# Kernel tuning notes

Measured on AMD Instinct MI355X. Metric: run time of the kernel, lower is better.

The kernel has to match this reference:

```python
import jax, jax.numpy as jnp
import numpy as np

H, W, BS, CIN = 224, 608, 1, 128
CLS = (16, 12, 10)
PAD = (0, 2, 3)
C12 = CLS[0] * CLS[1]            # 192
C123 = C12 * CLS[2]              # 1920
SUPER = 384
CFACT = C123 // SUPER            # 5
PAD_PROJ = 0.1


def _p(key, shape):
    return jax.random.normal(key, shape, dtype=jnp.float32) * 0.05


def setup_inputs() -> dict:
    key = jax.random.key(0)
    ks = iter(jax.random.split(key, 32))
    d = {"x_in": jax.random.normal(next(ks), (BS, CIN, H, W), dtype=jnp.float32)}
    # stage-1: grouped 1x1 convs (groups=height -> one [out,in] matmul per image line)
    for i, (ci, co) in enumerate([(32, 32), (32, 32), (32, CLS[0] + 2 * PAD[0])]):
        d[f"w1_{i}"] = _p(next(ks), (H, co, ci))
        d[f"b1_{i}"] = _p(next(ks), (H, co))
    # stage-2: CondMul tables indexed by line*16 + stage-1 class
    for i, (ci, co) in enumerate([(32, 32), (32, 32), (32, CLS[1] + 2 * PAD[1])]):
        d[f"w2_{i}"] = _p(next(ks), (H * CLS[0], ci, co))
        d[f"b2_{i}"] = _p(next(ks), (H * CLS[0], co))
    # stage-3: CondMul tables indexed by line*192 + stage-12 class
    for i, (ci, co) in enumerate([(32, 32), (32, 32), (32, CLS[2] + 2 * PAD[2])]):
        d[f"w3_{i}"] = _p(next(ks), (H * C12, ci, co))
        d[f"b3_{i}"] = _p(next(ks), (H * C12, co))
    d["wr0"] = _p(next(ks), (H * SUPER, 32, 32))
    d["br0"] = _p(next(ks), (H * SUPER, 32))
    d["wr1"] = _p(next(ks), (H * C123, 32, 1))
    d["br1"] = _p(next(ks), (H * C123, 1))
    return d


def _condmul(x, inds, w, b):
    # CondMul: y[n] = x[n] @ w[inds[n]] + b[inds[n]]
    return jnp.einsum('ni,nio->no', x, w[inds]) + b[inds]


def _forward(x_in, w1, b1, w2, b2, w3, b3, wr0, br0, wr1, br1):
    bs, _, h, w_ = x_in.shape
    lrelu = jax.nn.leaky_relu  # negative_slope=0.01, same as torch default
    offsets = jnp.arange(h, dtype=jnp.int32).reshape(1, 1, h, 1)
    # ---- stage 1: per-line 1x1 grouped conv stack -> argmax class
    x = x_in[:, 0:32].transpose(0, 2, 1, 3)                    # [b,h,32,w]
    for i in range(3):
        x = jnp.einsum('bhiw,hoi->bhow', x, w1[i]) + b1[i][None, :, :, None]
        if i < 2:
            x = lrelu(x)
    x = x.transpose(0, 2, 1, 3)                                 # [b,16,h,w]
    inds1 = jnp.argmax(x, axis=1)[:, None].astype(jnp.int32)    # [b,1,h,w]
    inds1_l = (inds1 + CLS[0] * offsets).reshape(-1)
    # ---- stage 2: CondMul chain conditioned on (line, class1)
    x = x_in[:, 32:64].transpose(0, 2, 3, 1).reshape(-1, 32)    # [N,32]
    for i in range(3):
        x = _condmul(x, inds1_l, w2[i], b2[i])
        if i < 2:
            x = lrelu(x)
    inds2 = jnp.argmax(x, axis=1).astype(jnp.int32).reshape(bs, 1, h, w_)
    inds12 = inds1 * CLS[1] + (inds2 - PAD[1])
    inds12_l = (jnp.clip(inds12, 0, C12 - 1) + C12 * offsets).reshape(-1)
    # ---- stage 3: CondMul chain conditioned on (line, class12)
    x = x_in[:, 64:96].transpose(0, 2, 3, 1).reshape(-1, 32)
    for i in range(3):
        if i < 2:
            x = lrelu(_condmul(x, inds12_l, w3[i], b3[i]))
        else:
            x = _condmul(x, inds12_l, w3[i], b3[i])
    inds3 = jnp.argmax(x, axis=1).astype(jnp.int32).reshape(bs, 1, h, w_)
    inds123 = jnp.clip(inds12 * CLS[2] + (inds3 - PAD[2]), 0, C123 - 1)
    inds = inds123.reshape(-1)
    lines = jnp.broadcast_to(offsets, (bs, 1, h, w_)).reshape(-1)
    inds_l = inds + C123 * lines                                 # per-leaf index
    inds_super_l = inds // CFACT + SUPER * lines                 # superclass index (reg_line_div=1)
    x = x_in[:, 96:128].transpose(0, 2, 3, 1).reshape(-1, 32)
    x = lrelu(_condmul(x, inds_super_l, wr0, br0))
    r = _condmul(x, inds_l, wr1, br1)[:, 0]                      # [N]
    out = (inds.astype(jnp.float32) + r).reshape(bs, 1, h, w_) / float(C123)
    out = (out - PAD_PROJ) / (1.0 - 2.0 * PAD_PROJ)              # undo projector padding
    return out


def reference(x_in, w1_0, b1_0, w1_1, b1_1, w1_2, b1_2,
              w2_0, b2_0, w2_1, b2_1, w2_2, b2_2,
              w3_0, b3_0, w3_1, b3_1, w3_2, b3_2,
              wr0, br0, wr1, br1):
    return _forward(x_in,
                    (w1_0, w1_1, w1_2), (b1_0, b1_1, b1_2),
                    (w2_0, w2_1, w2_2), (b2_0, b2_1, b2_2),
                    (w3_0, w3_1, w3_2), (b3_0, b3_1, b3_2),
                    wr0, br0, wr1, br1)
```

## Files before the change

### kernel.cpp

```cpp
#include <hip/hip_runtime.h>
#include <cstddef>

#define HH 224
#define WW 608
#define HWSZ (HH * WW)

__device__ __forceinline__ float lrelu(float v) { return v > 0.0f ? v : 0.01f * v; }

template <int CO>
__device__ __forceinline__ void cm4(const float* wmat,
                                    const float* bvec,
                                    int s, const float (&act)[8], float (&acc)[CO / 4]) {
    constexpr int CH = CO / 4;
#pragma unroll
    for (int j = 0; j < CH; j++) acc[j] = 0.0f;
#pragma unroll
    for (int sp = 0; sp < 4; sp++) {
#pragma unroll
        for (int ii = 0; ii < 8; ii++) {
            float xi = __shfl(act[ii], sp, 4);
            const float* wr = wmat + (sp * 8 + ii) * CO + s * CH;
            if constexpr (CH == 8) {
                float4 a = *reinterpret_cast<const float4*>(wr);
                float4 b = *reinterpret_cast<const float4*>(wr + 4);
                acc[0] = fmaf(xi, a.x, acc[0]); acc[1] = fmaf(xi, a.y, acc[1]);
                acc[2] = fmaf(xi, a.z, acc[2]); acc[3] = fmaf(xi, a.w, acc[3]);
                acc[4] = fmaf(xi, b.x, acc[4]); acc[5] = fmaf(xi, b.y, acc[5]);
                acc[6] = fmaf(xi, b.z, acc[6]); acc[7] = fmaf(xi, b.w, acc[7]);
            } else {
                float4 a = *reinterpret_cast<const float4*>(wr);
                acc[0] = fmaf(xi, a.x, acc[0]); acc[1] = fmaf(xi, a.y, acc[1]);
                acc[2] = fmaf(xi, a.z, acc[2]); acc[3] = fmaf(xi, a.w, acc[3]);
            }
        }
    }
#pragma unroll
    for (int j = 0; j < CH; j++) acc[j] += bvec[s * CH + j];
}

__device__ __forceinline__ void wb_lrelu8(float (&act)[8], const float (&acc)[8]) {
#pragma unroll
    for (int j = 0; j < 8; j++) act[j] = lrelu(acc[j]);
}

__device__ __forceinline__ int argmax4(const float (&v)[4], int s) {
    float bv = v[0];
    int bi = 4 * s;
#pragma unroll
    for (int j = 1; j < 4; j++) {
        if (v[j] > bv) { bv = v[j]; bi = 4 * s + j; }
    }
#pragma unroll
    for (int m = 1; m <= 2; m <<= 1) {
        float ov = __shfl_xor(bv, m, 4);
        int oi = __shfl_xor(bi, m, 4);
        if (ov > bv || (ov == bv && oi < bi)) { bv = ov; bi = oi; }
    }
    return bi;
}

template <int NF>
__device__ __forceinline__ void stage_mat(float* ws, const float* __restrict__ src, int lane) {
    const float4* s4 = reinterpret_cast<const float4*>(src);
    float4* w4 = reinterpret_cast<float4*>(ws);
#pragma unroll
    for (int t = 0; t < NF / 4 / 64; t++) w4[t * 64 + lane] = s4[t * 64 + lane];
}

extern "C" __global__ __launch_bounds__(256, 4)
void regressor_fused(const float* __restrict__ x_in,
                     const float* __restrict__ w1_0, const float* __restrict__ b1_0,
                     const float* __restrict__ w1_1, const float* __restrict__ b1_1,
                     const float* __restrict__ w1_2, const float* __restrict__ b1_2,
                     const float* __restrict__ w2_0, const float* __restrict__ b2_0,
                     const float* __restrict__ w2_1, const float* __restrict__ b2_1,
                     const float* __restrict__ w2_2, const float* __restrict__ b2_2,
                     const float* __restrict__ w3_0, const float* __restrict__ b3_0,
                     const float* __restrict__ w3_1, const float* __restrict__ b3_1,
                     const float* __restrict__ w3_2, const float* __restrict__ b3_2,
                     const float* __restrict__ wr0, const float* __restrict__ br0,
                     const float* __restrict__ wr1, const float* __restrict__ br1,
                     float* __restrict__ out) {
    const int h = blockIdx.y;
    const int tid = threadIdx.x;
    const int p = tid >> 2;
    const int s = tid & 3;
    const int lane = tid & 63;
    const int w = blockIdx.x * 64 + p;
    const bool valid = (w < WW);
    const int wc = valid ? w : (WW - 1);
    const int base = h * WW + wc;

    __shared__ __align__(16) float sW0[1024];
    __shared__ __align__(16) float sW1[1024];
    __shared__ __align__(16) float sW2[512];
    __shared__ __align__(16) float sUni[4][1024];
    float* ws = sUni[tid >> 6];

    for (int tt = tid; tt < 1024; tt += 256) {
        int i = tt >> 5, o = tt & 31;
        sW0[tt] = w1_0[h * 1024 + o * 32 + i];
        sW1[tt] = w1_1[h * 1024 + o * 32 + i];
    }
    for (int tt = tid; tt < 512; tt += 256) {
        int i = tt >> 4, o = tt & 15;
        sW2[tt] = w1_2[h * 512 + o * 32 + i];
    }
    __syncthreads();

    float act[8], acc8[8], acc4[4];

#pragma unroll
    for (int ii = 0; ii < 8; ii++) act[ii] = x_in[(8 * s + ii) * HWSZ + base];
    cm4<32>(sW0, b1_0 + h * 32, s, act, acc8);
    wb_lrelu8(act, acc8);
    cm4<32>(sW1, b1_1 + h * 32, s, act, acc8);
    wb_lrelu8(act, acc8);
    cm4<16>(sW2, b1_2 + h * 16, s, act, acc4);
    const int i1 = argmax4(acc4, s);

#pragma unroll
    for (int ii = 0; ii < 8; ii++) act[ii] = x_in[(32 + 8 * s + ii) * HWSZ + base];
    {
        const int fi1 = __builtin_amdgcn_readfirstlane(i1);
        if (__all(i1 == fi1)) {
            const size_t u = (size_t)h * 16 + (size_t)fi1;
            stage_mat<1024>(ws, w2_0 + u * 1024, lane);
            cm4<32>(ws, b2_0 + u * 32, s, act, acc8);
            wb_lrelu8(act, acc8);
            stage_mat<1024>(ws, w2_1 + u * 1024, lane);
            cm4<32>(ws, b2_1 + u * 32, s, act, acc8);
            wb_lrelu8(act, acc8);
            stage_mat<512>(ws, w2_2 + u * 512, lane);
            cm4<16>(ws, b2_2 + u * 16, s, act, acc4);
        } else {
            const size_t idx2 = (size_t)h * 16 + (size_t)i1;
            cm4<32>(w2_0 + idx2 * 1024, b2_0 + idx2 * 32, s, act, acc8);
            wb_lrelu8(act, acc8);
            cm4<32>(w2_1 + idx2 * 1024, b2_1 + idx2 * 32, s, act, acc8);
            wb_lrelu8(act, acc8);
            cm4<16>(w2_2 + idx2 * 512, b2_2 + idx2 * 16, s, act, acc4);
        }
    }
    const int i2 = argmax4(acc4, s);

    const int inds12 = i1 * 12 + (i2 - 2);
    const int c12 = min(max(inds12, 0), 191);

#pragma unroll
    for (int ii = 0; ii < 8; ii++) act[ii] = x_in[(64 + 8 * s + ii) * HWSZ + base];
    {
        const int fc12 = __builtin_amdgcn_readfirstlane(c12);
        if (__all(c12 == fc12)) {
            const size_t u = (size_t)h * 192 + (size_t)fc12;
            stage_mat<1024>(ws, w3_0 + u * 1024, lane);
            cm4<32>(ws, b3_0 + u * 32, s, act, acc8);
            wb_lrelu8(act, acc8);
            stage_mat<1024>(ws, w3_1 + u * 1024, lane);
            cm4<32>(ws, b3_1 + u * 32, s, act, acc8);
            wb_lrelu8(act, acc8);
            stage_mat<512>(ws, w3_2 + u * 512, lane);
            cm4<16>(ws, b3_2 + u * 16, s, act, acc4);
        } else {
            const size_t idx3 = (size_t)h * 192 + (size_t)c12;
            cm4<32>(w3_0 + idx3 * 1024, b3_0 + idx3 * 32, s, act, acc8);
            wb_lrelu8(act, acc8);
            cm4<32>(w3_1 + idx3 * 1024, b3_1 + idx3 * 32, s, act, acc8);
            wb_lrelu8(act, acc8);
            cm4<16>(w3_2 + idx3 * 512, b3_2 + idx3 * 16, s, act, acc4);
        }
    }
    const int i3 = argmax4(acc4, s);

    const int inds123 = min(max(inds12 * 10 + (i3 - 3), 0), 1919);

#pragma unroll
    for (int ii = 0; ii < 8; ii++) act[ii] = x_in[(96 + 8 * s + ii) * HWSZ + base];
    {
        const int sup = inds123 / 5;
        const int fsup = __builtin_amdgcn_readfirstlane(sup);
        if (__all(sup == fsup)) {
            const size_t u = (size_t)h * 384 + (size_t)fsup;
            stage_mat<1024>(ws, wr0 + u * 1024, lane);
            cm4<32>(ws, br0 + u * 32, s, act, acc8);
        } else {
            const size_t idxs = (size_t)h * 384 + (size_t)sup;
            cm4<32>(wr0 + idxs * 1024, br0 + idxs * 32, s, act, acc8);
        }
    }
    wb_lrelu8(act, acc8);

    const size_t idxr = (size_t)h * 1920 + (size_t)inds123;
    const float* __restrict__ wr1r = wr1 + idxr * 32 + 8 * s;
    float4 wa = *reinterpret_cast<const float4*>(wr1r);
    float4 wb = *reinterpret_cast<const float4*>(wr1r + 4);
    float rpart = 0.0f;
    rpart = fmaf(act[0], wa.x, rpart); rpart = fmaf(act[1], wa.y, rpart);
    rpart = fmaf(act[2], wa.z, rpart); rpart = fmaf(act[3], wa.w, rpart);
    rpart = fmaf(act[4], wb.x, rpart); rpart = fmaf(act[5], wb.y, rpart);
    rpart = fmaf(act[6], wb.z, rpart); rpart = fmaf(act[7], wb.w, rpart);
    rpart += __shfl_xor(rpart, 1, 4);
    rpart += __shfl_xor(rpart, 2, 4);
    const float r = rpart + br1[idxr];

    if (s == 0 && valid) {
        float v = ((float)inds123 + r) * (1.0f / 1920.0f);
        out[h * WW + w] = (v - 0.1f) * 1.25f;
    }
}

extern "C" void kernel_launch(void* const* d_in, const int* in_sizes, int n_in,
                              void* d_out, int out_size, void* d_ws, size_t ws_size,
                              hipStream_t stream) {
    const float* p[23];
    for (int i = 0; i < 23; i++) p[i] = (const float*)d_in[i];
    dim3 grid(10, HH);
    regressor_fused<<<grid, 256, 0, stream>>>(
        p[0],
        p[1], p[2], p[3], p[4], p[5], p[6],
        p[7], p[8], p[9], p[10], p[11], p[12],
        p[13], p[14], p[15], p[16], p[17], p[18],
        p[19], p[20], p[21], p[22],
        (float*)d_out);
}
```

Before: 126.3 us.

## Sort pixels by class within block before each conditional matmul stage

Before each CondMul stage, the block stages the stage's input activations in shared memory and computes a rank-sort permutation of its 64 pixels by class index. Threads then process pixels in sorted order, so each 16-pixel wavefront is more likely to share a single class and take the uniform shared-memory-staged weight path instead of divergent per-pixel global loads. The cost is several extra __syncthreads, an O(64^2) serial rank computation on 64 threads per stage, and more shared memory, which may lower occupancy.

```diff
diff --git a/kernel.cpp b/kernel.cpp
--- a/kernel.cpp
+++ b/kernel.cpp
@@ -95,6 +95,11 @@
     __shared__ __align__(16) float sW1[1024];
     __shared__ __align__(16) float sW2[512];
     __shared__ __align__(16) float sUni[4][1024];
+    __shared__ __align__(16) float xbuf[32][65];
+    __shared__ int skey[64];
+    __shared__ int sperm[64];
+    __shared__ int sraw[64];
+    __shared__ int sraw2[64];
     float* ws = sUni[tid >> 6];
 
     for (int tt = tid; tt < 1024; tt += 256) {
@@ -118,13 +123,30 @@
     wb_lrelu8(act, acc8);
     cm4<16>(sW2, b1_2 + h * 16, s, act, acc4);
     const int i1 = argmax4(acc4, s);
-
-#pragma unroll
-    for (int ii = 0; ii < 8; ii++) act[ii] = x_in[(32 + 8 * s + ii) * HWSZ + base];
+    if (s == 0) skey[p] = i1;
+
+#pragma unroll
+    for (int ii = 0; ii < 8; ii++)
+        xbuf[8 * s + ii][p] = x_in[(32 + 8 * s + ii) * HWSZ + base];
+    __syncthreads();
+    if (tid < 64) {
+        int k = skey[tid], rank = 0;
+        for (int j = 0; j < 64; j++) {
+            int kj = skey[j];
+            rank += (kj < k || (kj == k && j < tid)) ? 1 : 0;
+        }
+        sperm[rank] = tid;
+    }
+    __syncthreads();
+
     {
-        const int fi1 = __builtin_amdgcn_readfirstlane(i1);
-        if (__all(i1 == fi1)) {
-            const size_t u = (size_t)h * 16 + (size_t)fi1;
+        const int q = sperm[p];
+        const int i1q = skey[q];
+#pragma unroll
+        for (int ii = 0; ii < 8; ii++) act[ii] = xbuf[8 * s + ii][q];
+        const int fc = __builtin_amdgcn_readfirstlane(i1q);
+        if (__all(i1q == fc)) {
+            const size_t u = (size_t)h * 16 + (size_t)fc;
             stage_mat<1024>(ws, w2_0 + u * 1024, lane);
             cm4<32>(ws, b2_0 + u * 32, s, act, acc8);
             wb_lrelu8(act, acc8);
@@ -134,25 +156,42 @@
             stage_mat<512>(ws, w2_2 + u * 512, lane);
             cm4<16>(ws, b2_2 + u * 16, s, act, acc4);
         } else {
-            const size_t idx2 = (size_t)h * 16 + (size_t)i1;
+            const size_t idx2 = (size_t)h * 16 + (size_t)i1q;
             cm4<32>(w2_0 + idx2 * 1024, b2_0 + idx2 * 32, s, act, acc8);
             wb_lrelu8(act, acc8);
             cm4<32>(w2_1 + idx2 * 1024, b2_1 + idx2 * 32, s, act, acc8);
             wb_lrelu8(act, acc8);
             cm4<16>(w2_2 + idx2 * 512, b2_2 + idx2 * 16, s, act, acc4);
         }
-    }
-    const int i2 = argmax4(acc4, s);
-
-    const int inds12 = i1 * 12 + (i2 - 2);
-    const int c12 = min(max(inds12, 0), 191);
-
-#pragma unroll
-    for (int ii = 0; ii < 8; ii++) act[ii] = x_in[(64 + 8 * s + ii) * HWSZ + base];
+        const int i2 = argmax4(acc4, s);
+        if (s == 0) sraw[q] = i1q * 12 + (i2 - 2);
+    }
+    __syncthreads();
+
+#pragma unroll
+    for (int ii = 0; ii < 8; ii++)
+        xbuf[8 * s + ii][p] = x_in[(64 + 8 * s + ii) * HWSZ + base];
+    if (s == 0) skey[p] = min(max(sraw[p], 0), 191);
+    __syncthreads();
+    if (tid < 64) {
+        int k = skey[tid], rank = 0;
+        for (int j = 0; j < 64; j++) {
+            int kj = skey[j];
+            rank += (kj < k || (kj == k && j < tid)) ? 1 : 0;
+        }
+        sperm[rank] = tid;
+    }
+    __syncthreads();
+
     {
-        const int fc12 = __builtin_amdgcn_readfirstlane(c12);
-        if (__all(c12 == fc12)) {
-            const size_t u = (size_t)h * 192 + (size_t)fc12;
+        const int q = sperm[p];
+        const int r12 = sraw[q];
+        const int c12 = min(max(r12, 0), 191);
+#pragma unroll
+        for (int ii = 0; ii < 8; ii++) act[ii] = xbuf[8 * s + ii][q];
+        const int fc = __builtin_amdgcn_readfirstlane(c12);
+        if (__all(c12 == fc)) {
+            const size_t u = (size_t)h * 192 + (size_t)fc;
             stage_mat<1024>(ws, w3_0 + u * 1024, lane);
             cm4<32>(ws, b3_0 + u * 32, s, act, acc8);
             wb_lrelu8(act, acc8);
@@ -169,43 +208,61 @@
             wb_lrelu8(act, acc8);
             cm4<16>(w3_2 + idx3 * 512, b3_2 + idx3 * 16, s, act, acc4);
         }
-    }
-    const int i3 = argmax4(acc4, s);
-
-    const int inds123 = min(max(inds12 * 10 + (i3 - 3), 0), 1919);
-
-#pragma unroll
-    for (int ii = 0; ii < 8; ii++) act[ii] = x_in[(96 + 8 * s + ii) * HWSZ + base];
+        const int i3 = argmax4(acc4, s);
+        if (s == 0) sraw2[q] = min(max(r12 * 10 + (i3 - 3), 0), 1919);
+    }
+    __syncthreads();
+
+#pragma unroll
+    for (int ii = 0; ii < 8; ii++)
+        xbuf[8 * s + ii][p] = x_in[(96 + 8 * s + ii) * HWSZ + base];
+    if (s == 0) skey[p] = sraw2[p] / 5;
+    __syncthreads();
+    if (tid < 64) {
+        int k = skey[tid], rank = 0;
+        for (int j = 0; j < 64; j++) {
+            int kj = skey[j];
+            rank += (kj < k || (kj == k && j < tid)) ? 1 : 0;
+        }
+        sperm[rank] = tid;
+    }
+    __syncthreads();
+
     {
-        const int sup = inds123 / 5;
-        const int fsup = __builtin_amdgcn_readfirstlane(sup);
-        if (__all(sup == fsup)) {
-            const size_t u = (size_t)h * 384 + (size_t)fsup;
+        const int q = sperm[p];
+        const int leaf = sraw2[q];
+        const int sup = leaf / 5;
+#pragma unroll
+        for (int ii = 0; ii < 8; ii++) act[ii] = xbuf[8 * s + ii][q];
+        const int fc = __builtin_amdgcn_readfirstlane(sup);
+        if (__all(sup == fc)) {
+            const size_t u = (size_t)h * 384 + (size_t)fc;
             stage_mat<1024>(ws, wr0 + u * 1024, lane);
             cm4<32>(ws, br0 + u * 32, s, act, acc8);
         } else {
             const size_t idxs = (size_t)h * 384 + (size_t)sup;
             cm4<32>(wr0 + idxs * 1024, br0 + idxs * 32, s, act, acc8);
         }
-    }
-    wb_lrelu8(act, acc8);
-
-    const size_t idxr = (size_t)h * 1920 + (size_t)inds123;
-    const float* __restrict__ wr1r = wr1 + idxr * 32 + 8 * s;
-    float4 wa = *reinterpret_cast<const float4*>(wr1r);
-    float4 wb = *reinterpret_cast<const float4*>(wr1r + 4);
-    float rpart = 0.0f;
-    rpart = fmaf(act[0], wa.x, rpart); rpart = fmaf(act[1], wa.y, rpart);
-    rpart = fmaf(act[2], wa.z, rpart); rpart = fmaf(act[3], wa.w, rpart);
-    rpart = fmaf(act[4], wb.x, rpart); rpart = fmaf(act[5], wb.y, rpart);
-    rpart = fmaf(act[6], wb.z, rpart); rpart = fmaf(act[7], wb.w, rpart);
-    rpart += __shfl_xor(rpart, 1, 4);
-    rpart += __shfl_xor(rpart, 2, 4);
-    const float r = rpart + br1[idxr];
-
-    if (s == 0 && valid) {
-        float v = ((float)inds123 + r) * (1.0f / 1920.0f);
-        out[h * WW + w] = (v - 0.1f) * 1.25f;
+        wb_lrelu8(act, acc8);
+
+        const size_t idxr = (size_t)h * 1920 + (size_t)leaf;
+        const float* wr1r = wr1 + idxr * 32 + 8 * s;
+        float4 wa = *reinterpret_cast<const float4*>(wr1r);
+        float4 wb = *reinterpret_cast<const float4*>(wr1r + 4);
+        float rpart = 0.0f;
+        rpart = fmaf(act[0], wa.x, rpart); rpart = fmaf(act[1], wa.y, rpart);
+        rpart = fmaf(act[2], wa.z, rpart); rpart = fmaf(act[3], wa.w, rpart);
+        rpart = fmaf(act[4], wb.x, rpart); rpart = fmaf(act[5], wb.y, rpart);
+        rpart = fmaf(act[6], wb.z, rpart); rpart = fmaf(act[7], wb.w, rpart);
+        rpart += __shfl_xor(rpart, 1, 4);
+        rpart += __shfl_xor(rpart, 2, 4);
+        const float r = rpart + br1[idxr];
+
+        const int wq = blockIdx.x * 64 + q;
+        if (s == 0 && wq < WW) {
+            float v = ((float)leaf + r) * (1.0f / 1920.0f);
+            out[h * WW + wq] = (v - 0.1f) * 1.25f;
+        }
     }
 }
 
```

New measurement: 128.7 us. About the same (+1.9%).
